# Performance work log

Hardware: AMD Instinct MI355X
Metric: run time of the kernel (lower is better)

Reference implementation:

```python
import jax, jax.numpy as jnp
import numpy as np

B, C_IN, H, W = 32, 64, 64, 64
D, O, S_SP, K = 256, 512, 4, 3


def setup_inputs() -> dict:
    key = jax.random.key(0)
    k1, k2, k3, k4, k5 = jax.random.split(key, 5)
    x = jax.random.normal(k1, (B, C_IN, H, W), dtype=jnp.float32)
    dictionary = jax.random.normal(k2, (D, C_IN, K, K), dtype=jnp.float32)
    lookup_coefficients = jax.random.normal(k3, (O, S_SP), dtype=jnp.float32)
    bias = jax.random.normal(k4, (O,), dtype=jnp.float32)
    lookup_indices = jax.random.randint(k5, (O, S_SP), 0, D)
    return {
        "x": x,
        "dictionary": dictionary,
        "lookup_coefficients": lookup_coefficients,
        "bias": bias,
        "lookup_indices": lookup_indices,
    }


def reference(x, dictionary, lookup_coefficients, bias, lookup_indices):
    # Dictionary conv: S has shape [B, D, H, W] (stride 1, padding 1, 3x3 kernel)
    S = jax.lax.conv_general_dilated(
        x, dictionary,
        window_strides=(1, 1),
        padding=((1, 1), (1, 1)),
        dimension_numbers=("NCHW", "OIHW", "NCHW"),
    )
    # Build dense [O, D] combine matrix via scatter-add (duplicate indices
    # accumulate, matching the original += loop), then one GEMM.
    rows = jnp.arange(O)[:, None]  # [O, 1] broadcast against [O, sparsity]
    Wc = jnp.zeros((O, D), dtype=S.dtype).at[rows, lookup_indices].add(lookup_coefficients)
    out = jnp.einsum("bdhw,od->bohw", S, Wc)
    return out + bias[None, :, None, None]
```

## Files before the change

kernel.cpp:

```cpp
#include <hip/hip_runtime.h>
#include <stdint.h>

#define NB 32
#define NC 64
#define NH 64
#define NW 64
#define NO 512
#define HP 66

typedef __bf16 bf16x8 __attribute__((ext_vector_type(8)));
typedef short  s16x8  __attribute__((ext_vector_type(8)));
typedef float  f32x4  __attribute__((ext_vector_type(4)));

__device__ __forceinline__ uint16_t f2bf(float f) {
  uint32_t u = __builtin_bit_cast(uint32_t, f);
  u += 0x7fffu + ((u >> 16) & 1u);
  return (uint16_t)(u >> 16);
}

__device__ __forceinline__ void gld16(const uint16_t* g, uint16_t* l) {
  __builtin_amdgcn_global_load_lds(
      (const __attribute__((address_space(1))) void*)(g),
      (__attribute__((address_space(3))) void*)(l), 16, 0, 0);
}

__global__ void k_build_w(const float* __restrict__ dict,
                          const float* __restrict__ coef,
                          const int*   __restrict__ idx,
                          uint16_t*    __restrict__ Wl) {
  __shared__ float tmp[576];
  const int o = blockIdx.x;
  const int t = threadIdx.x;
  float v = 0.f;
#pragma unroll
  for (int s = 0; s < 4; ++s)
    v += coef[o * 4 + s] * dict[idx[o * 4 + s] * 576 + t];
  tmp[t] = v;
  __syncthreads();
  const int c = t & 63, p = t >> 6;
  const int sl = ((p * NO + o) * 8 + ((c >> 3) ^ (o & 7))) * 8 + (c & 7);
  Wl[sl] = f2bf(tmp[c * 9 + p]);
}

__global__ void k_nhwc(const float* __restrict__ x, uint16_t* __restrict__ xh) {
  const int bh = blockIdx.x;
  const int b = bh / HP, hp = bh % HP;
  const int t = threadIdx.x;
  uint16_t* row = xh + (size_t)(b * HP + hp) * 4096;
  if (hp == 0 || hp == HP - 1) {
    int4* r4 = reinterpret_cast<int4*>(row);
    r4[t]       = int4{0, 0, 0, 0};
    r4[t + 256] = int4{0, 0, 0, 0};
    return;
  }
  __shared__ float tile[64][65];
  const int h = hp - 1;
  const int w = t & 63;
#pragma unroll
  for (int c = (t >> 6); c < 64; c += 4)
    tile[c][w] = x[((size_t)(b * NC + c) * NH + h) * NW + w];
  __syncthreads();
#pragma unroll
  for (int i = 0; i < 2; ++i) {
    const int s = t + i * 256;
    const int w2 = s >> 3, cb = s & 7;
    uint32_t d[4];
#pragma unroll
    for (int j = 0; j < 4; ++j) {
      const uint32_t lo = f2bf(tile[cb * 8 + 2 * j][w2]);
      const uint32_t hi = f2bf(tile[cb * 8 + 2 * j + 1][w2]);
      d[j] = lo | (hi << 16);
    }
    reinterpret_cast<int4*>(row)[w2 * 8 + (cb ^ (w2 & 7))] =
        int4{(int)d[0], (int)d[1], (int)d[2], (int)d[3]};
  }
}

__global__ __launch_bounds__(512, 2) void k_conv(
    const uint16_t* __restrict__ xh,
    const uint16_t* __restrict__ Wl,
    const float*    __restrict__ bias,
    float*          __restrict__ out) {
  __shared__ __align__(16) uint16_t xs[10 * 66 * 64];
  __shared__ __align__(16) uint16_t as[9 * 64 * 64];

  const int t = threadIdx.x;
  const int flat = blockIdx.x;
  const int s    = (flat & 7) * 256 + (flat >> 3);
  const int ot   = s & 7;
  const int gy   = s >> 3;
  const int o0 = ot * 64;
  const int b  = gy >> 3;
  const int h0 = (gy & 7) * 8;

  const int lane = t & 63;
  const int wid  = t >> 6;

  if (t < 160) {
    const int r = t >> 4, sl = (t >> 3) & 1, j = t & 7;
    reinterpret_cast<int4*>(xs)[r * 528 + sl * 520 + j] = int4{0, 0, 0, 0};
  }

  {
    const uint16_t* srow = xh + (size_t)(b * HP + h0 + wid) * 4096;
    uint16_t* drow = xs + wid * 4224 + 64;
#pragma unroll
    for (int k = 0; k < 8; ++k)
      gld16(srow + k * 512 + lane * 8, drow + k * 512);
    const int r2 = 8 + (wid >> 2);
    const int kb = (wid & 3) * 2;
    const uint16_t* srow2 = xh + (size_t)(b * HP + h0 + r2) * 4096;
    uint16_t* drow2 = xs + r2 * 4224 + 64;
    gld16(srow2 + kb * 512 + lane * 8, drow2 + kb * 512);
    gld16(srow2 + (kb + 1) * 512 + lane * 8, drow2 + (kb + 1) * 512);
  }

  {
#pragma unroll
    for (int j = 0; j < 9; ++j) {
      const int c = wid * 9 + j;
      const int tap = c >> 3, k = c & 7;
      const uint16_t* src =
          Wl + (size_t)tap * 32768 + o0 * 64 + k * 512;
      gld16(src + lane * 8, as + tap * 4096 + k * 512);
    }
  }

  const int wn  = wid;
  const int l15 = lane & 15;
  const int lg  = lane >> 4;

  f32x4 acc[4][4];
#pragma unroll
  for (int pb = 0; pb < 4; ++pb)
#pragma unroll
    for (int ob = 0; ob < 4; ++ob)
      acc[pb][ob] = (f32x4){0.f, 0.f, 0.f, 0.f};
  float bvv[4];
#pragma unroll
  for (int ob = 0; ob < 4; ++ob)
    bvv[ob] = bias[o0 + ob * 16 + l15];

  __syncthreads();

#pragma unroll
  for (int g = 0; g < 3; ++g) {
    const int dw = g - 1;
#pragma unroll
    for (int q = 0; q < 2; ++q) {
      const int cbB = (q * 4 + lg) ^ ((l15 + dw) & 7);
      const uint16_t* xb = xs + (l15 + dw + 1) * 64 + cbB * 8;
      const int cbA = (q * 4 + lg) ^ (l15 & 7);
      const uint16_t* ab = as + l15 * 64 + cbA * 8;
#pragma unroll
      for (int dh = 0; dh < 3; ++dh) {
        const int tap = dh * 3 + g;
        bf16x8 braw[4], af[4];
#pragma unroll
        for (int nw = 0; nw < 4; ++nw)
          braw[nw] = __builtin_bit_cast(bf16x8,
              *reinterpret_cast<const s16x8*>(
                  xb + (wn + dh) * 4224 + nw * 1024));
#pragma unroll
        for (int ob = 0; ob < 4; ++ob)
          af[ob] = __builtin_bit_cast(bf16x8,
              *reinterpret_cast<const s16x8*>(
                  ab + tap * 4096 + ob * 1024));
#pragma unroll
        for (int pb = 0; pb < 4; ++pb)
#pragma unroll
          for (int ob = 0; ob < 4; ++ob)
            acc[pb][ob] = __builtin_amdgcn_mfma_f32_16x16x32_bf16(
                braw[pb], af[ob], acc[pb][ob], 0, 0, 0);
      }
    }
  }

  const int h = h0 + wn;
#pragma unroll
  for (int pb = 0; pb < 4; ++pb) {
#pragma unroll
    for (int ob = 0; ob < 4; ++ob) {
      const int o = o0 + ob * 16 + l15;
      f32x4 v = acc[pb][ob];
      const float bv = bvv[ob];
      v[0] += bv; v[1] += bv; v[2] += bv; v[3] += bv;
      float* dst = out + ((size_t)(b * NO + o) * NH + h) * NW +
                   pb * 16 + lg * 4;
      __builtin_nontemporal_store(v, reinterpret_cast<f32x4*>(dst));
    }
  }
}

extern "C" void kernel_launch(void* const* d_in, const int* in_sizes, int n_in,
                              void* d_out, int out_size, void* d_ws, size_t ws_size,
                              hipStream_t stream) {
  const float* x    = (const float*)d_in[0];
  const float* dict = (const float*)d_in[1];
  const float* coef = (const float*)d_in[2];
  const float* bias = (const float*)d_in[3];
  const int*   idx  = (const int*)d_in[4];
  float* out = (float*)d_out;

  uint16_t* xh = (uint16_t*)d_ws;
  uint16_t* Wl = (uint16_t*)((char*)d_ws + (18u << 20));

  hipLaunchKernelGGL(k_build_w, dim3(NO), dim3(576), 0, stream, dict, coef, idx, Wl);
  hipLaunchKernelGGL(k_nhwc, dim3(NB * HP), dim3(256), 0, stream, x, xh);
  hipLaunchKernelGGL(k_conv, dim3(2048), dim3(512), 0, stream, xh, Wl, bias, out);
}
```

Measured before the change: 111.2 us.

## Restructure conv into double-buffered per-tap pipeline with larger 256x256 tiles

The conv kernel is reorganised into a 256-output by 256-pixel tile per block (4 rows) with 8 warps in a 2x4 layout. It iterates over the 9 taps with double-buffered LDS staging of weight and shifted input slices, issuing the next tap's loads before computing the current one. The NHWC pre-pass now writes width-padded rows (66 columns), so input staging is plain contiguous copies and the in-kernel padding zeroing goes away. This aims to overlap global loads with MFMA and raise arithmetic intensity per block, at the cost of more accumulator registers (128 floats per lane) and fewer blocks.

```diff
diff --git a/kernel.cpp b/kernel.cpp
--- a/kernel.cpp
+++ b/kernel.cpp
@@ -6,7 +6,6 @@
 #define NH 64
 #define NW 64
 #define NO 512
-#define HP 66
 
 typedef __bf16 bf16x8 __attribute__((ext_vector_type(8)));
 typedef short  s16x8  __attribute__((ext_vector_type(8)));
@@ -44,13 +43,12 @@
 
 __global__ void k_nhwc(const float* __restrict__ x, uint16_t* __restrict__ xh) {
   const int bh = blockIdx.x;
-  const int b = bh / HP, hp = bh % HP;
+  const int b = bh / 66, hp = bh % 66;
   const int t = threadIdx.x;
-  uint16_t* row = xh + (size_t)(b * HP + hp) * 4096;
-  if (hp == 0 || hp == HP - 1) {
-    int4* r4 = reinterpret_cast<int4*>(row);
-    r4[t]       = int4{0, 0, 0, 0};
-    r4[t + 256] = int4{0, 0, 0, 0};
+  uint16_t* row = xh + (size_t)(b * 66 + hp) * 4224;
+  int4* r4 = reinterpret_cast<int4*>(row);
+  if (hp == 0 || hp == 65) {
+    for (int j = t; j < 528; j += 256) r4[j] = int4{0, 0, 0, 0};
     return;
   }
   __shared__ float tile[64][65];
@@ -60,10 +58,13 @@
   for (int c = (t >> 6); c < 64; c += 4)
     tile[c][w] = x[((size_t)(b * NC + c) * NH + h) * NW + w];
   __syncthreads();
+  if (t < 16)
+    r4[(t >> 3) * 520 + (t & 7)] = int4{0, 0, 0, 0};
 #pragma unroll
   for (int i = 0; i < 2; ++i) {
     const int s = t + i * 256;
     const int w2 = s >> 3, cb = s & 7;
+    const int wp = w2 + 1;
     uint32_t d[4];
 #pragma unroll
     for (int j = 0; j < 4; ++j) {
@@ -71,7 +72,7 @@
       const uint32_t hi = f2bf(tile[cb * 8 + 2 * j + 1][w2]);
       d[j] = lo | (hi << 16);
     }
-    reinterpret_cast<int4*>(row)[w2 * 8 + (cb ^ (w2 & 7))] =
+    r4[wp * 8 + (cb ^ (wp & 7))] =
         int4{(int)d[0], (int)d[1], (int)d[2], (int)d[3]};
   }
 }
@@ -81,98 +82,98 @@
     const uint16_t* __restrict__ Wl,
     const float*    __restrict__ bias,
     float*          __restrict__ out) {
-  __shared__ __align__(16) uint16_t xs[10 * 66 * 64];
-  __shared__ __align__(16) uint16_t as[9 * 64 * 64];
+  __shared__ __align__(16) uint16_t lds[4 * 16384];
 
   const int t = threadIdx.x;
-  const int flat = blockIdx.x;
-  const int s    = (flat & 7) * 256 + (flat >> 3);
-  const int ot   = s & 7;
-  const int gy   = s >> 3;
-  const int o0 = ot * 64;
-  const int b  = gy >> 3;
-  const int h0 = (gy & 7) * 8;
-
   const int lane = t & 63;
   const int wid  = t >> 6;
-
-  if (t < 160) {
-    const int r = t >> 4, sl = (t >> 3) & 1, j = t & 7;
-    reinterpret_cast<int4*>(xs)[r * 528 + sl * 520 + j] = int4{0, 0, 0, 0};
-  }
-
-  {
-    const uint16_t* srow = xh + (size_t)(b * HP + h0 + wid) * 4096;
-    uint16_t* drow = xs + wid * 4224 + 64;
-#pragma unroll
-    for (int k = 0; k < 8; ++k)
-      gld16(srow + k * 512 + lane * 8, drow + k * 512);
-    const int r2 = 8 + (wid >> 2);
-    const int kb = (wid & 3) * 2;
-    const uint16_t* srow2 = xh + (size_t)(b * HP + h0 + r2) * 4096;
-    uint16_t* drow2 = xs + r2 * 4224 + 64;
-    gld16(srow2 + kb * 512 + lane * 8, drow2 + kb * 512);
-    gld16(srow2 + (kb + 1) * 512 + lane * 8, drow2 + (kb + 1) * 512);
-  }
-
-  {
-#pragma unroll
-    for (int j = 0; j < 9; ++j) {
-      const int c = wid * 9 + j;
-      const int tap = c >> 3, k = c & 7;
-      const uint16_t* src =
-          Wl + (size_t)tap * 32768 + o0 * 64 + k * 512;
-      gld16(src + lane * 8, as + tap * 4096 + k * 512);
-    }
-  }
-
-  const int wn  = wid;
+  const int flat = blockIdx.x;
+  const int s    = (flat & 7) * 128 + (flat >> 3);
+  const int mt   = s & 1;
+  const int pt   = s >> 1;
+  const int O0 = mt * 256;
+  const int b  = pt >> 4;
+  const int h0 = (pt & 15) * 4;
+
+  const int wm  = wid & 1;
+  const int wn  = wid >> 1;
   const int l15 = lane & 15;
   const int lg  = lane >> 4;
 
-  f32x4 acc[4][4];
+  auto stageA = [&](int k) {
+    uint16_t* dst = lds + ((2 * k) & 3) * 16384;
+    const uint16_t* src = Wl + ((size_t)k * NO + O0) * 64;
+#pragma unroll
+    for (int j = 0; j < 4; ++j) {
+      const int ch = wid * 4 + j;
+      gld16(src + ch * 512 + lane * 8, dst + ch * 512);
+    }
+  };
+  auto stageB = [&](int k) {
+    uint16_t* dst = lds + ((2 * k + 1) & 3) * 16384;
+    const int dh = k / 3, dwp = k % 3;
+#pragma unroll
+    for (int j = 0; j < 4; ++j) {
+      const int ch = wid * 4 + j;
+      const int r = ch >> 3, oc = ch & 7;
+      const uint16_t* src =
+          xh + ((size_t)(b * 66) + h0 + r + dh) * 4224 + (dwp + oc * 8) * 64;
+      gld16(src + lane * 8, dst + ch * 512);
+    }
+  };
+
+  float bvv[8];
+#pragma unroll
+  for (int ob = 0; ob < 8; ++ob)
+    bvv[ob] = bias[O0 + wm * 128 + ob * 16 + l15];
+
+  f32x4 acc[4][8];
 #pragma unroll
   for (int pb = 0; pb < 4; ++pb)
 #pragma unroll
-    for (int ob = 0; ob < 4; ++ob)
+    for (int ob = 0; ob < 8; ++ob)
       acc[pb][ob] = (f32x4){0.f, 0.f, 0.f, 0.f};
-  float bvv[4];
-#pragma unroll
-  for (int ob = 0; ob < 4; ++ob)
-    bvv[ob] = bias[o0 + ob * 16 + l15];
-
-  __syncthreads();
-
-#pragma unroll
-  for (int g = 0; g < 3; ++g) {
-    const int dw = g - 1;
+
+  stageA(0);
+  stageB(0);
+
+#pragma unroll
+  for (int k = 0; k < 9; ++k) {
+    if (k > 0)
+      asm volatile("s_barrier" ::: "memory");
+    if (k < 8) { stageA(k + 1); stageB(k + 1); }
+    if (k < 8)
+      asm volatile("s_waitcnt vmcnt(8)\n\ts_barrier" ::: "memory");
+    else
+      asm volatile("s_waitcnt vmcnt(0)\n\ts_barrier" ::: "memory");
+
+    const uint16_t* As = lds + ((2 * k) & 3) * 16384;
+    const uint16_t* Bs = lds + ((2 * k + 1) & 3) * 16384;
+    const int dwp = k % 3;
+
 #pragma unroll
     for (int q = 0; q < 2; ++q) {
-      const int cbB = (q * 4 + lg) ^ ((l15 + dw) & 7);
-      const uint16_t* xb = xs + (l15 + dw + 1) * 64 + cbB * 8;
       const int cbA = (q * 4 + lg) ^ (l15 & 7);
-      const uint16_t* ab = as + l15 * 64 + cbA * 8;
-#pragma unroll
-      for (int dh = 0; dh < 3; ++dh) {
-        const int tap = dh * 3 + g;
-        bf16x8 braw[4], af[4];
-#pragma unroll
-        for (int nw = 0; nw < 4; ++nw)
-          braw[nw] = __builtin_bit_cast(bf16x8,
-              *reinterpret_cast<const s16x8*>(
-                  xb + (wn + dh) * 4224 + nw * 1024));
-#pragma unroll
-        for (int ob = 0; ob < 4; ++ob)
-          af[ob] = __builtin_bit_cast(bf16x8,
-              *reinterpret_cast<const s16x8*>(
-                  ab + tap * 4096 + ob * 1024));
-#pragma unroll
-        for (int pb = 0; pb < 4; ++pb)
-#pragma unroll
-          for (int ob = 0; ob < 4; ++ob)
-            acc[pb][ob] = __builtin_amdgcn_mfma_f32_16x16x32_bf16(
-                braw[pb], af[ob], acc[pb][ob], 0, 0, 0);
-      }
+      const int cbB = (q * 4 + lg) ^ ((l15 + dwp) & 7);
+      bf16x8 af[8], braw[4];
+#pragma unroll
+      for (int ob = 0; ob < 8; ++ob)
+        af[ob] = __builtin_bit_cast(bf16x8,
+            *reinterpret_cast<const s16x8*>(
+                As + (wm * 128 + ob * 16 + l15) * 64 + cbA * 8));
+#pragma unroll
+      for (int pb = 0; pb < 4; ++pb)
+        braw[pb] = __builtin_bit_cast(bf16x8,
+            *reinterpret_cast<const s16x8*>(
+                Bs + (wn * 64 + pb * 16 + l15) * 64 + cbB * 8));
+      __builtin_amdgcn_s_setprio(1);
+#pragma unroll
+      for (int pb = 0; pb < 4; ++pb)
+#pragma unroll
+        for (int ob = 0; ob < 8; ++ob)
+          acc[pb][ob] = __builtin_amdgcn_mfma_f32_16x16x32_bf16(
+              braw[pb], af[ob], acc[pb][ob], 0, 0, 0);
+      __builtin_amdgcn_s_setprio(0);
     }
   }
 
@@ -180,8 +181,8 @@
 #pragma unroll
   for (int pb = 0; pb < 4; ++pb) {
 #pragma unroll
-    for (int ob = 0; ob < 4; ++ob) {
-      const int o = o0 + ob * 16 + l15;
+    for (int ob = 0; ob < 8; ++ob) {
+      const int o = O0 + wm * 128 + ob * 16 + l15;
       f32x4 v = acc[pb][ob];
       const float bv = bvv[ob];
       v[0] += bv; v[1] += bv; v[2] += bv; v[3] += bv;
@@ -206,6 +207,6 @@
   uint16_t* Wl = (uint16_t*)((char*)d_ws + (18u << 20));
 
   hipLaunchKernelGGL(k_build_w, dim3(NO), dim3(576), 0, stream, dict, coef, idx, Wl);
-  hipLaunchKernelGGL(k_nhwc, dim3(NB * HP), dim3(256), 0, stream, x, xh);
-  hipLaunchKernelGGL(k_conv, dim3(2048), dim3(512), 0, stream, xh, Wl, bias, out);
-}
+  hipLaunchKernelGGL(k_nhwc, dim3(NB * 66), dim3(256), 0, stream, x, xh);
+  hipLaunchKernelGGL(k_conv, dim3(1024), dim3(512), 0, stream, xh, Wl, bias, out);
+}
```

Result: slower. 133.8 us (+20.4%).

## Loop conv blocks over all output tiles and merge prep kernels

Applied to the files above, without the earlier changes.

Each conv block now keeps its input patch in LDS and loops over all 8 output-channel tiles, using two alternating accumulator sets. The next weight tile is staged into LDS after a barrier while the current tile's results are stored. The two preprocessing kernels are fused into one launch. This removes the repeated input-patch staging of the old 2048-block grid and one kernel launch. In exchange the grid shrinks to 256 blocks (about one per CU), which costs parallelism and latency hiding. It also adds serializing barriers, and the hand-set vmcnt waits are fragile.

```diff
diff --git a/kernel.cpp b/kernel.cpp
--- a/kernel.cpp
+++ b/kernel.cpp
@@ -24,31 +24,45 @@
       (__attribute__((address_space(3))) void*)(l), 16, 0, 0);
 }
 
-__global__ void k_build_w(const float* __restrict__ dict,
-                          const float* __restrict__ coef,
-                          const int*   __restrict__ idx,
-                          uint16_t*    __restrict__ Wl) {
-  __shared__ float tmp[576];
-  const int o = blockIdx.x;
+__global__ void k_prep(const float* __restrict__ dict,
+                       const float* __restrict__ coef,
+                       const int*   __restrict__ idx,
+                       const float* __restrict__ x,
+                       uint16_t*    __restrict__ Wl,
+                       uint16_t*    __restrict__ xh) {
+  const int bid = blockIdx.x;
   const int t = threadIdx.x;
-  float v = 0.f;
-#pragma unroll
-  for (int s = 0; s < 4; ++s)
-    v += coef[o * 4 + s] * dict[idx[o * 4 + s] * 576 + t];
-  tmp[t] = v;
-  __syncthreads();
-  const int c = t & 63, p = t >> 6;
-  const int sl = ((p * NO + o) * 8 + ((c >> 3) ^ (o & 7))) * 8 + (c & 7);
-  Wl[sl] = f2bf(tmp[c * 9 + p]);
-}
-
-__global__ void k_nhwc(const float* __restrict__ x, uint16_t* __restrict__ xh) {
-  const int bh = blockIdx.x;
+  if (bid < NO) {
+    __shared__ float tmp[576];
+    const int o = bid;
+#pragma unroll
+    for (int j = 0; j < 3; ++j) {
+      const int id = t + j * 256;
+      if (id < 576) {
+        float v = 0.f;
+#pragma unroll
+        for (int s = 0; s < 4; ++s)
+          v += coef[o * 4 + s] * dict[idx[o * 4 + s] * 576 + id];
+        tmp[id] = v;
+      }
+    }
+    __syncthreads();
+#pragma unroll
+    for (int j = 0; j < 3; ++j) {
+      const int id = t + j * 256;
+      if (id < 576) {
+        const int c = id & 63, p = id >> 6;
+        const int sl = ((p * NO + o) * 8 + ((c >> 3) ^ (o & 7))) * 8 + (c & 7);
+        Wl[sl] = f2bf(tmp[c * 9 + p]);
+      }
+    }
+    return;
+  }
+  const int bh = bid - NO;
   const int b = bh / HP, hp = bh % HP;
-  const int t = threadIdx.x;
   uint16_t* row = xh + (size_t)(b * HP + hp) * 4096;
+  int4* r4 = reinterpret_cast<int4*>(row);
   if (hp == 0 || hp == HP - 1) {
-    int4* r4 = reinterpret_cast<int4*>(row);
     r4[t]       = int4{0, 0, 0, 0};
     r4[t + 256] = int4{0, 0, 0, 0};
     return;
@@ -71,7 +85,7 @@
       const uint32_t hi = f2bf(tile[cb * 8 + 2 * j + 1][w2]);
       d[j] = lo | (hi << 16);
     }
-    reinterpret_cast<int4*>(row)[w2 * 8 + (cb ^ (w2 & 7))] =
+    r4[w2 * 8 + (cb ^ (w2 & 7))] =
         int4{(int)d[0], (int)d[1], (int)d[2], (int)d[3]};
   }
 }
@@ -85,22 +99,17 @@
   __shared__ __align__(16) uint16_t as[9 * 64 * 64];
 
   const int t = threadIdx.x;
-  const int flat = blockIdx.x;
-  const int s    = (flat & 7) * 256 + (flat >> 3);
-  const int ot   = s & 7;
-  const int gy   = s >> 3;
-  const int o0 = ot * 64;
+  const int lane = t & 63;
+  const int wid  = t >> 6;
+  const int blk = blockIdx.x;
+  const int gy = (blk & 7) * 32 + (blk >> 3);
   const int b  = gy >> 3;
   const int h0 = (gy & 7) * 8;
-
-  const int lane = t & 63;
-  const int wid  = t >> 6;
 
   if (t < 160) {
     const int r = t >> 4, sl = (t >> 3) & 1, j = t & 7;
     reinterpret_cast<int4*>(xs)[r * 528 + sl * 520 + j] = int4{0, 0, 0, 0};
   }
-
   {
     const uint16_t* srow = xh + (size_t)(b * HP + h0 + wid) * 4096;
     uint16_t* drow = xs + wid * 4224 + 64;
@@ -114,82 +123,104 @@
     gld16(srow2 + kb * 512 + lane * 8, drow2 + kb * 512);
     gld16(srow2 + (kb + 1) * 512 + lane * 8, drow2 + (kb + 1) * 512);
   }
-
-  {
+  auto stage_a = [&](int ot) {
 #pragma unroll
     for (int j = 0; j < 9; ++j) {
       const int c = wid * 9 + j;
       const int tap = c >> 3, k = c & 7;
-      const uint16_t* src =
-          Wl + (size_t)tap * 32768 + o0 * 64 + k * 512;
+      const uint16_t* src = Wl + (size_t)tap * 32768 + (ot * 64) * 64 + k * 512;
       gld16(src + lane * 8, as + tap * 4096 + k * 512);
     }
-  }
+  };
+  stage_a(0);
 
   const int wn  = wid;
   const int l15 = lane & 15;
   const int lg  = lane >> 4;
 
-  f32x4 acc[4][4];
-#pragma unroll
-  for (int pb = 0; pb < 4; ++pb)
+  float bvv[8][4];
+#pragma unroll
+  for (int ot = 0; ot < 8; ++ot)
 #pragma unroll
     for (int ob = 0; ob < 4; ++ob)
-      acc[pb][ob] = (f32x4){0.f, 0.f, 0.f, 0.f};
-  float bvv[4];
-#pragma unroll
-  for (int ob = 0; ob < 4; ++ob)
-    bvv[ob] = bias[o0 + ob * 16 + l15];
+      bvv[ot][ob] = bias[ot * 64 + ob * 16 + l15];
+
+  f32x4 accA[4][4], accB[4][4];
 
   __syncthreads();
 
-#pragma unroll
-  for (int g = 0; g < 3; ++g) {
-    const int dw = g - 1;
-#pragma unroll
-    for (int q = 0; q < 2; ++q) {
-      const int cbB = (q * 4 + lg) ^ ((l15 + dw) & 7);
-      const uint16_t* xb = xs + (l15 + dw + 1) * 64 + cbB * 8;
-      const int cbA = (q * 4 + lg) ^ (l15 & 7);
-      const uint16_t* ab = as + l15 * 64 + cbA * 8;
-#pragma unroll
-      for (int dh = 0; dh < 3; ++dh) {
-        const int tap = dh * 3 + g;
-        bf16x8 braw[4], af[4];
-#pragma unroll
-        for (int nw = 0; nw < 4; ++nw)
-          braw[nw] = __builtin_bit_cast(bf16x8,
-              *reinterpret_cast<const s16x8*>(
-                  xb + (wn + dh) * 4224 + nw * 1024));
-#pragma unroll
-        for (int ob = 0; ob < 4; ++ob)
-          af[ob] = __builtin_bit_cast(bf16x8,
-              *reinterpret_cast<const s16x8*>(
-                  ab + tap * 4096 + ob * 1024));
-#pragma unroll
-        for (int pb = 0; pb < 4; ++pb)
-#pragma unroll
-          for (int ob = 0; ob < 4; ++ob)
-            acc[pb][ob] = __builtin_amdgcn_mfma_f32_16x16x32_bf16(
-                braw[pb], af[ob], acc[pb][ob], 0, 0, 0);
-      }
-    }
-  }
-
   const int h = h0 + wn;
-#pragma unroll
-  for (int pb = 0; pb < 4; ++pb) {
-#pragma unroll
-    for (int ob = 0; ob < 4; ++ob) {
-      const int o = o0 + ob * 16 + l15;
-      f32x4 v = acc[pb][ob];
-      const float bv = bvv[ob];
-      v[0] += bv; v[1] += bv; v[2] += bv; v[3] += bv;
-      float* dst = out + ((size_t)(b * NO + o) * NH + h) * NW +
-                   pb * 16 + lg * 4;
-      __builtin_nontemporal_store(v, reinterpret_cast<f32x4*>(dst));
-    }
-  }
+
+#define ROUND(ACC, OT) do {                                                  \
+    _Pragma("unroll")                                                        \
+    for (int pb = 0; pb < 4; ++pb)                                           \
+      _Pragma("unroll")                                                      \
+      for (int ob = 0; ob < 4; ++ob)                                         \
+        ACC[pb][ob] = (f32x4){0.f, 0.f, 0.f, 0.f};                           \
+    _Pragma("unroll")                                                        \
+    for (int g = 0; g < 3; ++g) {                                            \
+      const int dw = g - 1;                                                  \
+      _Pragma("unroll")                                                      \
+      for (int q = 0; q < 2; ++q) {                                          \
+        const int cbB = (q * 4 + lg) ^ ((l15 + dw) & 7);                     \
+        const uint16_t* xb = xs + (l15 + dw + 1) * 64 + cbB * 8;             \
+        const int cbA = (q * 4 + lg) ^ (l15 & 7);                            \
+        const uint16_t* ab = as + l15 * 64 + cbA * 8;                        \
+        _Pragma("unroll")                                                    \
+        for (int dh = 0; dh < 3; ++dh) {                                     \
+          const int tap = dh * 3 + g;                                        \
+          bf16x8 braw[4], af[4];                                             \
+          _Pragma("unroll")                                                  \
+          for (int nw = 0; nw < 4; ++nw)                                     \
+            braw[nw] = __builtin_bit_cast(bf16x8,                            \
+                *reinterpret_cast<const s16x8*>(                             \
+                    xb + (wn + dh) * 4224 + nw * 1024));                     \
+          _Pragma("unroll")                                                  \
+          for (int ob = 0; ob < 4; ++ob)                                     \
+            af[ob] = __builtin_bit_cast(bf16x8,                              \
+                *reinterpret_cast<const s16x8*>(                             \
+                    ab + tap * 4096 + ob * 1024));                           \
+          _Pragma("unroll")                                                  \
+          for (int pb = 0; pb < 4; ++pb)                                     \
+            _Pragma("unroll")                                                \
+            for (int ob = 0; ob < 4; ++ob)                                   \
+              ACC[pb][ob] = __builtin_amdgcn_mfma_f32_16x16x32_bf16(         \
+                  braw[pb], af[ob], ACC[pb][ob], 0, 0, 0);                   \
+        }                                                                    \
+      }                                                                      \
+    }                                                                        \
+       \
+    asm volatile("s_waitcnt lgkmcnt(0)" ::: "memory");                       \
+    __builtin_amdgcn_s_barrier();                                            \
+    asm volatile("" ::: "memory");                                           \
+    if ((OT) < 7) stage_a((OT) + 1);                   \
+    asm volatile("" ::: "memory");                                           \
+    _Pragma("unroll")                                                        \
+    for (int pb = 0; pb < 4; ++pb) {                                         \
+      _Pragma("unroll")                                                      \
+      for (int ob = 0; ob < 4; ++ob) {                                       \
+        const int o = (OT) * 64 + ob * 16 + l15;                             \
+        f32x4 v = ACC[pb][ob];                                               \
+        const float bv = bvv[(OT)][ob];                                      \
+        v[0] += bv; v[1] += bv; v[2] += bv; v[3] += bv;                      \
+        float* dst = out + ((size_t)(b * NO + o) * NH + h) * NW +            \
+                     pb * 16 + lg * 4;                                       \
+        __builtin_nontemporal_store(v, reinterpret_cast<f32x4*>(dst));       \
+      }                                                                      \
+    }                                                                        \
+    asm volatile("" ::: "memory");                                           \
+    if ((OT) < 7) {                                                          \
+      asm volatile("s_waitcnt vmcnt(16)" ::: "memory");   \
+      __builtin_amdgcn_s_barrier();                                          \
+    }                                                                        \
+  } while (0)
+
+#pragma unroll
+  for (int o2 = 0; o2 < 4; ++o2) {
+    ROUND(accA, o2 * 2);
+    ROUND(accB, o2 * 2 + 1);
+  }
+#undef ROUND
 }
 
 extern "C" void kernel_launch(void* const* d_in, const int* in_sizes, int n_in,
@@ -205,7 +236,8 @@
   uint16_t* xh = (uint16_t*)d_ws;
   uint16_t* Wl = (uint16_t*)((char*)d_ws + (18u << 20));
 
-  hipLaunchKernelGGL(k_build_w, dim3(NO), dim3(576), 0, stream, dict, coef, idx, Wl);
-  hipLaunchKernelGGL(k_nhwc, dim3(NB * HP), dim3(256), 0, stream, x, xh);
-  hipLaunchKernelGGL(k_conv, dim3(2048), dim3(512), 0, stream, xh, Wl, bias, out);
-}
+  hipLaunchKernelGGL(k_prep, dim3(NO + NB * HP), dim3(256), 0, stream,
+                     dict, coef, idx, x, Wl, xh);
+  hipLaunchKernelGGL(k_conv, dim3(256), dim3(512), 0, stream,
+                     xh, Wl, bias, out);
+}
```

Result: no change. 109.3 us (-1.7%).
